# Performance work log

Hardware: AMD Instinct MI355X
Metric: run time of the kernel (lower is better)

## Reference

```python
import jax, jax.numpy as jnp
import numpy as np

SEQ_LEN = 4096
N_FEAT = 2048
N_PADD = 128


def setup_inputs() -> dict:
    key = jax.random.key(0)
    kx, kw = jax.random.split(key)
    x = jax.random.normal(kx, (SEQ_LEN, N_FEAT), dtype=jnp.float32)
    # Fused QKV dense: features = 3 * n_feat
    W = jax.random.normal(kw, (N_FEAT, 3 * N_FEAT), dtype=jnp.float32) * (1.0 / np.sqrt(N_FEAT))
    b = jnp.zeros((3 * N_FEAT,), dtype=jnp.float32)
    return {"x": x, "W": W, "b": b, "n_padd": N_PADD}


def reference(x, W, b, n_padd):
    # Fused QKV projection, split along feature axis (as in nn.Dense + jnp.split)
    qkv = x @ W + b  # [S, 3F]
    q, k, v = jnp.split(qkv, 3, axis=1)  # each [S, F]
    S, F = q.shape
    idx = jnp.arange(S)
    # scores[i, j] = q_i . k_j / sqrt(F)
    scores = (q @ k.T) * (1.0 / jnp.sqrt(jnp.float32(F)))  # [S, S]
    seq_mask = idx >= n_padd                      # valid (non-padding) positions
    causal = idx[None, :] <= idx[:, None]         # j <= i
    mask = causal & seq_mask[None, :]             # kernel: causal_mask & seq_mask
    row_valid = seq_mask                          # rows < n_padd are not computed/stored
    neg_inf = jnp.float32(-jnp.inf)
    scores = jnp.where(mask, scores, neg_inf)
    # Fully-masked (padding) rows would softmax to NaN; neutralize then zero output.
    scores = jnp.where(row_valid[:, None], scores, 0.0)
    att = jax.nn.softmax(scores, axis=-1)         # row-wise stable softmax
    out = att @ v                                 # [S, F]
    out = jnp.where(row_valid[:, None], out, 0.0)  # padded rows produce zeros
    return out
```

## Files before the change

kernel.cpp:

```cpp
#include <hip/hip_runtime.h>
#include <cstdint>
#include <cstddef>

typedef unsigned short u16;
typedef short v8s __attribute__((ext_vector_type(8)));
typedef float v4f __attribute__((ext_vector_type(4)));

constexpr int SEQ = 4096;
constexpr int FEAT = 2048;
constexpr int F3 = 6144;


__device__ __forceinline__ u16 f2bf(float f) {
  union { float f; uint32_t u; } v; v.f = f;
  uint32_t r = v.u + 0x7FFFu + ((v.u >> 16) & 1u);
  return (u16)(r >> 16);
}

__device__ __forceinline__ float bf2f(u16 s) {
  union { uint32_t u; float f; } v; v.u = ((uint32_t)s) << 16;
  return v.f;
}

__device__ __forceinline__ void gld_lds16(const u16* g, u16* l) {
  __builtin_amdgcn_global_load_lds(
      (const __attribute__((address_space(1))) void*)g,
      (__attribute__((address_space(3))) void*)l, 16, 0, 0);
}


__global__ void cvt_f32_bf16(const float* __restrict__ in, u16* __restrict__ out, int n8) {
  int i = blockIdx.x * 256 + threadIdx.x;
  if (i >= n8) return;
  const float4* p = (const float4*)in + (size_t)i * 2;
  float4 a = p[0], b = p[1];
  union { u16 s[8]; uint4 v; } u;
  u.s[0] = f2bf(a.x); u.s[1] = f2bf(a.y); u.s[2] = f2bf(a.z); u.s[3] = f2bf(a.w);
  u.s[4] = f2bf(b.x); u.s[5] = f2bf(b.y); u.s[6] = f2bf(b.z); u.s[7] = f2bf(b.w);
  *(uint4*)(out + (size_t)i * 8) = u.v;
}

__global__ void transp_f2b(const float* __restrict__ in, int ldin,
                           u16* __restrict__ out, int ldout) {
  __shared__ float tile[32][33];
  int c0 = blockIdx.x * 32, r0 = blockIdx.y * 32;
  int tx = threadIdx.x, ty = threadIdx.y;
#pragma unroll
  for (int p = 0; p < 4; ++p)
    tile[ty + 8 * p][tx] = in[(size_t)(r0 + ty + 8 * p) * ldin + c0 + tx];
  __syncthreads();
#pragma unroll
  for (int p = 0; p < 4; ++p)
    out[(size_t)(c0 + ty + 8 * p) * ldout + r0 + tx] = f2bf(tile[tx][ty + 8 * p]);
}

__global__ void transp_b2b(const u16* __restrict__ in, int ldin,
                           u16* __restrict__ out, int ldout) {
  __shared__ u16 tile[32][33];
  int c0 = blockIdx.x * 32, r0 = blockIdx.y * 32;
  int tx = threadIdx.x, ty = threadIdx.y;
#pragma unroll
  for (int p = 0; p < 4; ++p)
    tile[ty + 8 * p][tx] = in[(size_t)(r0 + ty + 8 * p) * ldin + c0 + tx];
  __syncthreads();
#pragma unroll
  for (int p = 0; p < 4; ++p)
    out[(size_t)(c0 + ty + 8 * p) * ldout + r0 + tx] = tile[tx][ty + 8 * p];
}

template<int OUTBF, int ADDB, int MODE>
__global__ __launch_bounds__(256) void gemm_bt(
    const u16* __restrict__ A, int lda,
    const u16* __restrict__ B, int ldb,
    void* __restrict__ Cv, int ldc,
    int K, const float* __restrict__ bias, float scale) {
  int bi, bj, ks, ke;
  if (MODE == 1) {
    const int t = blockIdx.x;
    bi = (int)((sqrtf(8.f * t + 1.f) - 1.f) * 0.5f);
    while ((bi + 1) * (bi + 2) / 2 <= t) ++bi;
    while (bi * (bi + 1) / 2 > t) --bi;
    bj = t - bi * (bi + 1) / 2;
    const int half = K >> 1;
    ks = blockIdx.z * half; ke = ks + half;
    Cv = (void*)((u16*)Cv + (size_t)blockIdx.z * SEQ * SEQ);
  } else if (MODE == 2) {
    bi = blockIdx.y; bj = blockIdx.x;
    const int half = (bi + 1) * 64;
    ks = blockIdx.z * half; ke = ks + half;
  } else {
    bi = blockIdx.y; bj = blockIdx.x;
    ks = 0; ke = K;
  }
  const int i0 = bi * 128, j0 = bj * 128;

  __shared__ u16 As[128 * 64];
  __shared__ u16 Bs[128 * 64];

  const int t = threadIdx.x;
  const int w = t >> 6, l = t & 63;
  const int wr = w >> 1, wc = w & 1;
  const int lm = l & 15, lq = l >> 4;
  const int lqs = ((lq + (lm >> 1)) & 3) * 8;

  v4f acc[4][4];
#pragma unroll
  for (int a = 0; a < 4; ++a)
#pragma unroll
    for (int b = 0; b < 4; ++b)
      acc[a][b] = v4f{0.f, 0.f, 0.f, 0.f};

  const int c1 = t + 256;
  const int r0c = t >> 2, o0 = ((((t & 3) - ((t >> 3) & 3)) & 3)) * 8;
  const int r1c = c1 >> 2, o1 = ((((c1 & 3) - ((c1 >> 3) & 3)) & 3)) * 8;
  const u16* Ag0 = A + (size_t)(i0 + r0c) * lda + o0;
  const u16* Ag1 = A + (size_t)(i0 + r1c) * lda + o1;
  const u16* Bg0 = B + (size_t)(j0 + r0c) * ldb + o0;
  const u16* Bg1 = B + (size_t)(j0 + r1c) * ldb + o1;
  u16* Al0 = &As[w * 512];
  u16* Al1 = &As[w * 512 + 2048];
  u16* Bl0 = &Bs[w * 512];
  u16* Bl1 = &Bs[w * 512 + 2048];

  for (int k0 = ks; k0 < ke; k0 += 64) {
    gld_lds16(Ag0 + k0, Al0);
    gld_lds16(Ag1 + k0, Al1);
    gld_lds16(Bg0 + k0, Bl0);
    gld_lds16(Bg1 + k0, Bl1);
    gld_lds16(Ag0 + k0 + 32, Al0 + 4096);
    gld_lds16(Ag1 + k0 + 32, Al1 + 4096);
    gld_lds16(Bg0 + k0 + 32, Bl0 + 4096);
    gld_lds16(Bg1 + k0 + 32, Bl1 + 4096);
    __syncthreads();

#pragma unroll
    for (int s = 0; s < 2; ++s) {
      v8s af[4], bfr[4];
#pragma unroll
      for (int mi = 0; mi < 4; ++mi)
        af[mi] = *(const v8s*)&As[s * 4096 + (wr * 64 + mi * 16 + lm) * 32 + lqs];
#pragma unroll
      for (int ni = 0; ni < 4; ++ni)
        bfr[ni] = *(const v8s*)&Bs[s * 4096 + (wc * 64 + ni * 16 + lm) * 32 + lqs];
#pragma unroll
      for (int mi = 0; mi < 4; ++mi)
#pragma unroll
        for (int ni = 0; ni < 4; ++ni)
          acc[mi][ni] = __builtin_amdgcn_mfma_f32_16x16x32_bf16(af[mi], bfr[ni], acc[mi][ni], 0, 0, 0);
    }
    __syncthreads();
  }

#pragma unroll
  for (int mi = 0; mi < 4; ++mi) {
#pragma unroll
    for (int ni = 0; ni < 4; ++ni) {
      const int cc = j0 + wc * 64 + ni * 16 + lm;
      const float badd = ADDB ? bias[cc] : 0.f;
#pragma unroll
      for (int r = 0; r < 4; ++r) {
        const int rr = i0 + wr * 64 + mi * 16 + lq * 4 + r;
        float v = acc[mi][ni][r] * scale + badd;
        if (OUTBF)           ((u16*)Cv)[(size_t)rr * ldc + cc] = f2bf(v);
        else if (MODE == 2)  atomicAdd((float*)Cv + (size_t)rr * ldc + cc, v);
        else                 ((float*)Cv)[(size_t)rr * ldc + cc] = v;
      }
    }
  }
}

__global__ __launch_bounds__(256) void softmax_rows(
    const u16* __restrict__ S0, const u16* __restrict__ S1,
    u16* __restrict__ att, const int* __restrict__ npad_p) {
  const int i = blockIdx.x;
  const int np = *npad_p;
  const int kend = ((i >> 7) + 1) << 7;
  const u16* r0 = S0 + (size_t)i * SEQ;
  const u16* r1 = S1 + (size_t)i * SEQ;
  u16* arow = att + (size_t)i * SEQ;
  const int t = threadIdx.x;

  float m = -3.0e38f, s = 0.f;
  for (int j = np + t; j <= i; j += 256) {
    float v = bf2f(r0[j]) + bf2f(r1[j]);
    if (v > m) { s = s * __expf(m - v) + 1.f; m = v; }
    else       { s += __expf(v - m); }
  }
#pragma unroll
  for (int off = 32; off > 0; off >>= 1) {
    float mo = __shfl_xor(m, off);
    float so = __shfl_xor(s, off);
    float M = fmaxf(m, mo);
    s = s * __expf(m - M) + so * __expf(mo - M);
    m = M;
  }
  __shared__ float sm[4], ss[4];
  const int w = t >> 6, l = t & 63;
  if (l == 0) { sm[w] = m; ss[w] = s; }
  __syncthreads();
  const float M = fmaxf(fmaxf(sm[0], sm[1]), fmaxf(sm[2], sm[3]));
  const float Ssum = ss[0] * __expf(sm[0] - M) + ss[1] * __expf(sm[1] - M) +
                     ss[2] * __expf(sm[2] - M) + ss[3] * __expf(sm[3] - M);
  const float inv = 1.f / Ssum;

  for (int j0b = t * 8; j0b < kend; j0b += 2048) {
    union { u16 s8[8]; uint4 v; } u;
#pragma unroll
    for (int q = 0; q < 8; ++q) {
      const int j = j0b + q;
      float a = 0.f;
      if (j >= np && j <= i)
        a = __expf(bf2f(r0[j]) + bf2f(r1[j]) - M) * inv;
      u.s8[q] = f2bf(a);
    }
    *(uint4*)(arow + j0b) = u.v;
  }
}


extern "C" void kernel_launch(void* const* d_in, const int* in_sizes, int n_in,
                              void* d_out, int out_size, void* d_ws, size_t ws_size,
                              hipStream_t stream) {
  const float* x = (const float*)d_in[0];
  const float* W = (const float*)d_in[1];
  const float* b = (const float*)d_in[2];
  const int* npad = (const int*)d_in[3];
  float* out = (float*)d_out;

  char* p = (char*)d_ws;
  u16* xb = (u16*)p;
  u16* Wt = (u16*)(p + (size_t)SEQ * FEAT * 2);
  u16* att = (u16*)p;
  p += (size_t)SEQ * FEAT * 2 + (size_t)F3 * FEAT * 2;
  u16* qkvb = (u16*)p;  p += (size_t)SEQ * F3 * 2;
  u16* vt   = (u16*)p;  p += (size_t)FEAT * SEQ * 2;
  u16* sc0  = (u16*)p;  p += (size_t)SEQ * SEQ * 2;
  u16* sc1  = (u16*)p;  p += (size_t)SEQ * SEQ * 2;
  if (ws_size < (size_t)(p - (char*)d_ws)) return;

  const float scale = 0.02209708691207961f;

  hipMemsetAsync(d_out, 0, (size_t)SEQ * FEAT * sizeof(float), stream);

  cvt_f32_bf16<<<SEQ * FEAT / 8 / 256, 256, 0, stream>>>(x, xb, SEQ * FEAT / 8);
  transp_f2b<<<dim3(F3 / 32, FEAT / 32), dim3(32, 8), 0, stream>>>(W, F3, Wt, FEAT);
  gemm_bt<1, 1, 0><<<dim3(F3 / 128, SEQ / 128), 256, 0, stream>>>(
      xb, FEAT, Wt, FEAT, (void*)qkvb, F3, FEAT, b, 1.0f);
  transp_b2b<<<dim3(FEAT / 32, SEQ / 32), dim3(32, 8), 0, stream>>>(
      qkvb + 2 * FEAT, F3, vt, SEQ);
  gemm_bt<1, 0, 1><<<dim3(32 * 33 / 2, 1, 2), 256, 0, stream>>>(
      qkvb, F3, qkvb + FEAT, F3, (void*)sc0, SEQ, FEAT, nullptr, scale);
  softmax_rows<<<SEQ, 256, 0, stream>>>(sc0, sc1, att, npad);
  gemm_bt<0, 0, 2><<<dim3(FEAT / 128, SEQ / 128, 2), 256, 0, stream>>>(
      att, SEQ, vt, SEQ, (void*)out, FEAT, 0, nullptr, 1.0f);
}
```

Baseline: 411.8 us.

## Switch GEMMs to 32x32x16 MFMA and replace atomic split-K with partial reduce

All GEMM variants now use the 32x32x16 bf16 MFMA with a 2x2 tile per wave instead of 4x4 16x16 tiles, reducing LDS fragment reads per MFMA. The final split-K attention-times-V GEMM writes two separate fp32 partials into the freed score buffer and a new kernel sums them. This removes the output memset and the float atomics, but adds an extra elementwise pass over the output.

```diff
diff --git a/kernel.cpp b/kernel.cpp
--- a/kernel.cpp
+++ b/kernel.cpp
@@ -4,7 +4,7 @@
 
 typedef unsigned short u16;
 typedef short v8s __attribute__((ext_vector_type(8)));
-typedef float v4f __attribute__((ext_vector_type(4)));
+typedef float v16f __attribute__((ext_vector_type(16)));
 
 constexpr int SEQ = 4096;
 constexpr int FEAT = 2048;
@@ -66,6 +66,16 @@
 #pragma unroll
   for (int p = 0; p < 4; ++p)
     out[(size_t)(c0 + ty + 8 * p) * ldout + r0 + tx] = tile[tx][ty + 8 * p];
+}
+
+__global__ void reduce_add(const float* __restrict__ p0, const float* __restrict__ p1,
+                           float* __restrict__ out, int n4) {
+  int i = blockIdx.x * 256 + threadIdx.x;
+  if (i >= n4) return;
+  float4 a = ((const float4*)p0)[i];
+  float4 b = ((const float4*)p1)[i];
+  float4 r; r.x = a.x + b.x; r.y = a.y + b.y; r.z = a.z + b.z; r.w = a.w + b.w;
+  ((float4*)out)[i] = r;
 }
 
 template<int OUTBF, int ADDB, int MODE>
@@ -88,6 +98,7 @@
     bi = blockIdx.y; bj = blockIdx.x;
     const int half = (bi + 1) * 64;
     ks = blockIdx.z * half; ke = ks + half;
+    Cv = (void*)((float*)Cv + (size_t)blockIdx.z * SEQ * FEAT);
   } else {
     bi = blockIdx.y; bj = blockIdx.x;
     ks = 0; ke = K;
@@ -100,15 +111,17 @@
   const int t = threadIdx.x;
   const int w = t >> 6, l = t & 63;
   const int wr = w >> 1, wc = w & 1;
-  const int lm = l & 15, lq = l >> 4;
-  const int lqs = ((lq + (lm >> 1)) & 3) * 8;
-
-  v4f acc[4][4];
-#pragma unroll
-  for (int a = 0; a < 4; ++a)
-#pragma unroll
-    for (int b = 0; b < 4; ++b)
-      acc[a][b] = v4f{0.f, 0.f, 0.f, 0.f};
+  const int ln31 = l & 31, lk = l >> 5;
+  const int swl = (ln31 >> 1) & 3;
+
+  v16f acc[2][2];
+#pragma unroll
+  for (int a = 0; a < 2; ++a)
+#pragma unroll
+    for (int b = 0; b < 2; ++b)
+#pragma unroll
+      for (int r = 0; r < 16; ++r)
+        acc[a][b][r] = 0.f;
 
   const int c1 = t + 256;
   const int r0c = t >> 2, o0 = ((((t & 3) - ((t >> 3) & 3)) & 3)) * 8;
@@ -135,35 +148,42 @@
 
 #pragma unroll
     for (int s = 0; s < 2; ++s) {
-      v8s af[4], bfr[4];
-#pragma unroll
-      for (int mi = 0; mi < 4; ++mi)
-        af[mi] = *(const v8s*)&As[s * 4096 + (wr * 64 + mi * 16 + lm) * 32 + lqs];
-#pragma unroll
-      for (int ni = 0; ni < 4; ++ni)
-        bfr[ni] = *(const v8s*)&Bs[s * 4096 + (wc * 64 + ni * 16 + lm) * 32 + lqs];
-#pragma unroll
-      for (int mi = 0; mi < 4; ++mi)
-#pragma unroll
-        for (int ni = 0; ni < 4; ++ni)
-          acc[mi][ni] = __builtin_amdgcn_mfma_f32_16x16x32_bf16(af[mi], bfr[ni], acc[mi][ni], 0, 0, 0);
+#pragma unroll
+      for (int kk = 0; kk < 2; ++kk) {
+        v8s af[2], bfr[2];
+#pragma unroll
+        for (int mi = 0; mi < 2; ++mi) {
+          const int R = wr * 64 + mi * 32 + ln31;
+          af[mi] = *(const v8s*)&As[s * 4096 + R * 32 + ((kk * 2 + lk + swl) & 3) * 8];
+        }
+#pragma unroll
+        for (int ni = 0; ni < 2; ++ni) {
+          const int R = wc * 64 + ni * 32 + ln31;
+          bfr[ni] = *(const v8s*)&Bs[s * 4096 + R * 32 + ((kk * 2 + lk + swl) & 3) * 8];
+        }
+#pragma unroll
+        for (int mi = 0; mi < 2; ++mi)
+#pragma unroll
+          for (int ni = 0; ni < 2; ++ni)
+            acc[mi][ni] = __builtin_amdgcn_mfma_f32_32x32x16_bf16(
+                af[mi], bfr[ni], acc[mi][ni], 0, 0, 0);
+      }
     }
     __syncthreads();
   }
 
 #pragma unroll
-  for (int mi = 0; mi < 4; ++mi) {
-#pragma unroll
-    for (int ni = 0; ni < 4; ++ni) {
-      const int cc = j0 + wc * 64 + ni * 16 + lm;
+  for (int mi = 0; mi < 2; ++mi) {
+#pragma unroll
+    for (int ni = 0; ni < 2; ++ni) {
+      const int cc = j0 + wc * 64 + ni * 32 + ln31;
       const float badd = ADDB ? bias[cc] : 0.f;
 #pragma unroll
-      for (int r = 0; r < 4; ++r) {
-        const int rr = i0 + wr * 64 + mi * 16 + lq * 4 + r;
-        float v = acc[mi][ni][r] * scale + badd;
-        if (OUTBF)           ((u16*)Cv)[(size_t)rr * ldc + cc] = f2bf(v);
-        else if (MODE == 2)  atomicAdd((float*)Cv + (size_t)rr * ldc + cc, v);
-        else                 ((float*)Cv)[(size_t)rr * ldc + cc] = v;
+      for (int reg = 0; reg < 16; ++reg) {
+        const int rr = i0 + wr * 64 + mi * 32 + (reg & 3) + 8 * (reg >> 2) + 4 * lk;
+        float v = acc[mi][ni][reg] * scale + badd;
+        if (OUTBF) ((u16*)Cv)[(size_t)rr * ldc + cc] = f2bf(v);
+        else       ((float*)Cv)[(size_t)rr * ldc + cc] = v;
       }
     }
   }
@@ -236,11 +256,10 @@
   u16* vt   = (u16*)p;  p += (size_t)FEAT * SEQ * 2;
   u16* sc0  = (u16*)p;  p += (size_t)SEQ * SEQ * 2;
   u16* sc1  = (u16*)p;  p += (size_t)SEQ * SEQ * 2;
+  float* op = (float*)sc0;
   if (ws_size < (size_t)(p - (char*)d_ws)) return;
 
   const float scale = 0.02209708691207961f;
-
-  hipMemsetAsync(d_out, 0, (size_t)SEQ * FEAT * sizeof(float), stream);
 
   cvt_f32_bf16<<<SEQ * FEAT / 8 / 256, 256, 0, stream>>>(x, xb, SEQ * FEAT / 8);
   transp_f2b<<<dim3(F3 / 32, FEAT / 32), dim3(32, 8), 0, stream>>>(W, F3, Wt, FEAT);
@@ -252,5 +271,7 @@
       qkvb, F3, qkvb + FEAT, F3, (void*)sc0, SEQ, FEAT, nullptr, scale);
   softmax_rows<<<SEQ, 256, 0, stream>>>(sc0, sc1, att, npad);
   gemm_bt<0, 0, 2><<<dim3(FEAT / 128, SEQ / 128, 2), 256, 0, stream>>>(
-      att, SEQ, vt, SEQ, (void*)out, FEAT, 0, nullptr, 1.0f);
-}
+      att, SEQ, vt, SEQ, (void*)op, FEAT, 0, nullptr, 1.0f);
+  reduce_add<<<SEQ * FEAT / 4 / 256, 256, 0, stream>>>(
+      op, op + (size_t)SEQ * FEAT, out, SEQ * FEAT / 4);
+}
```

Measured after the change: 427.2 us. 3.7% more time.
